# Kernel optimization log

Hardware: AMD Instinct MI355X
Metric: run time of the kernel (lower is better)

## Reference

```python
import jax, jax.numpy as jnp
import numpy as np

B, N, D, H = 4, 1024, 1024, 16
DH = D // H
MLP = 4 * D
EPS = 1e-6


def setup_inputs() -> dict:
    key = jax.random.key(0)
    ks = jax.random.split(key, 16)
    s = lambda fan_in: 1.0 / np.sqrt(fan_in)
    inp = {
        "x": jax.random.normal(ks[0], (B, N, D), jnp.float32),
        "c": jax.random.normal(ks[1], (B, D), jnp.float32),
        # weights stored (in, out); torch Linear is x @ W.T + b
        "Wq": jax.random.normal(ks[2], (D, D), jnp.float32) * s(D),
        "bq": jnp.zeros((D,), jnp.float32),
        "Wkv": jax.random.normal(ks[3], (D, 2 * D), jnp.float32) * s(D),
        "bkv": jnp.zeros((2 * D,), jnp.float32),
        "Wo": jax.random.normal(ks[4], (D, D), jnp.float32) * s(D),
        "bo": jnp.zeros((D,), jnp.float32),
        "W1": jax.random.normal(ks[5], (D, MLP), jnp.float32) * s(D),
        "b1": jnp.zeros((MLP,), jnp.float32),
        "W2": jax.random.normal(ks[6], (MLP, D), jnp.float32) * s(MLP),
        "b2": jnp.zeros((D,), jnp.float32),
        "Wada": jax.random.normal(ks[7], (D, 6 * D), jnp.float32) * s(D),
        "bada": jnp.zeros((6 * D,), jnp.float32),
    }
    return inp


def _layernorm(h):
    mu = jnp.mean(h, axis=-1, keepdims=True)
    var = jnp.mean(jnp.square(h - mu), axis=-1, keepdims=True)
    return (h - mu) / jnp.sqrt(var + EPS)


def _modulate(h, shift, scale):
    return h * (1.0 + scale[:, None, :]) + shift[:, None, :]


def reference(x, c, Wq, bq, Wkv, bkv, Wo, bo, W1, b1, W2, b2, Wada, bada):
    scale = DH ** -0.5
    mod = jax.nn.silu(c) @ Wada + bada  # [B, 6D]
    sh_msa, sc_msa, g_msa, sh_mlp, sc_mlp, g_mlp = jnp.split(mod, 6, axis=-1)

    # --- attention branch ---
    h = _modulate(_layernorm(x), sh_msa, sc_msa)
    q = (h @ Wq + bq).reshape(B, N, H, DH)
    kv = h @ Wkv + bkv
    k, v = jnp.split(kv, 2, axis=-1)
    k = k.reshape(B, N, H, DH)
    v = v.reshape(B, N, H, DH)
    sim = jnp.einsum("bihd,bjhd->bhij", q, k) * scale  # [B,H,N,N]
    attn = jax.nn.softmax(sim, axis=-1)
    out = jnp.einsum("bhij,bjhd->bihd", attn, v).reshape(B, N, D)
    out = out @ Wo + bo
    x = x + g_msa[:, None, :] * out

    # --- MLP branch ---
    h2 = _modulate(_layernorm(x), sh_mlp, sc_mlp)
    m = jax.nn.gelu(h2 @ W1 + b1, approximate=True) @ W2 + b2
    x = x + g_mlp[:, None, :] * m
    return x
```

## Files before the change

### kernel.cpp

```cpp
#include <hip/hip_runtime.h>
#include <hip/hip_bf16.h>
#include <cstdint>

typedef __attribute__((ext_vector_type(4))) float f32x4;
typedef __attribute__((ext_vector_type(16))) float f32x16;
typedef __attribute__((ext_vector_type(8))) short s16x8;
typedef __attribute__((ext_vector_type(4))) unsigned u32x4;
typedef unsigned short u16;

#define B_  4
#define N_  1024
#define D_  1024
#define H_  16
#define DH_ 64
#define M_  4096
#define SIXD 6144

__device__ __forceinline__ u16 f2bf(float f) {
    unsigned u = __builtin_bit_cast(unsigned, f);
    unsigned r = (u + 0x7fffu + ((u >> 16) & 1u)) >> 16;
    return (u16)r;
}

__device__ __forceinline__ unsigned cvtpk(float a, float b) {
    unsigned r;
    asm("v_cvt_pk_bf16_f32 %0, %1, %2" : "=v"(r) : "v"(a), "v"(b));
    return r;
}

__device__ __forceinline__ void gload16(const void* g, void* l) {
    __builtin_amdgcn_global_load_lds((const __attribute__((address_space(1))) void*)g,
                                     (__attribute__((address_space(3))) void*)l,
                                     16, 0, 0);
}

__global__ __launch_bounds__(256) void transpose_w(const float* __restrict__ in,
                                                   u16* __restrict__ out, int R, int C) {
    __shared__ float t[32][33];
    int tx = threadIdx.x & 31, ty = threadIdx.x >> 5;
    int r0 = blockIdx.y * 32, c0 = blockIdx.x * 32;
#pragma unroll
    for (int i = 0; i < 4; ++i)
        t[ty + 8 * i][tx] = in[(size_t)(r0 + ty + 8 * i) * C + c0 + tx];
    __syncthreads();
#pragma unroll
    for (int i = 0; i < 4; ++i)
        out[(size_t)(c0 + ty + 8 * i) * R + r0 + tx] = f2bf(t[tx][ty + 8 * i]);
}

__global__ __launch_bounds__(256) void modk(const float* __restrict__ c,
                                            const float* __restrict__ Wada,
                                            const float* __restrict__ bada,
                                            float* __restrict__ mod) {
    __shared__ float sc[D_];
    int b = blockIdx.y, tid = threadIdx.x;
    for (int i = tid; i < D_; i += 256) {
        float v = c[b * D_ + i];
        sc[i] = v / (1.f + __expf(-v));
    }
    __syncthreads();
    int col = blockIdx.x * 256 + tid;
    float a0 = 0.f, a1 = 0.f, a2 = 0.f, a3 = 0.f;
    for (int k = 0; k < D_; k += 4) {
        a0 = fmaf(sc[k + 0], Wada[(size_t)(k + 0) * SIXD + col], a0);
        a1 = fmaf(sc[k + 1], Wada[(size_t)(k + 1) * SIXD + col], a1);
        a2 = fmaf(sc[k + 2], Wada[(size_t)(k + 2) * SIXD + col], a2);
        a3 = fmaf(sc[k + 3], Wada[(size_t)(k + 3) * SIXD + col], a3);
    }
    mod[b * SIXD + col] = bada[col] + ((a0 + a1) + (a2 + a3));
}

__global__ __launch_bounds__(256) void ln_mod(const float* __restrict__ x,
                                              const float* __restrict__ mod,
                                              int shift_c, int scale_c,
                                              u16* __restrict__ h) {
    int row = blockIdx.x;
    int b = row >> 10;
    int tid = threadIdx.x, w = tid >> 6;
    float4 xv = ((const float4*)(x + (size_t)row * D_))[tid];
    float s  = xv.x + xv.y + xv.z + xv.w;
    float s2 = xv.x * xv.x + xv.y * xv.y + xv.z * xv.z + xv.w * xv.w;
#pragma unroll
    for (int m = 1; m <= 32; m <<= 1) { s += __shfl_xor(s, m); s2 += __shfl_xor(s2, m); }
    __shared__ float red[8];
    if ((tid & 63) == 0) { red[w * 2] = s; red[w * 2 + 1] = s2; }
    __syncthreads();
    float S  = red[0] + red[2] + red[4] + red[6];
    float S2 = red[1] + red[3] + red[5] + red[7];
    float mu = S * (1.f / D_);
    float var = S2 * (1.f / D_) - mu * mu;
    float rstd = rsqrtf(var + 1e-6f);
    int d0 = tid * 4;
    float4 shv = *(const float4*)(mod + b * SIXD + shift_c * D_ + d0);
    float4 scv = *(const float4*)(mod + b * SIXD + scale_c * D_ + d0);
    ushort4 o;
    o.x = f2bf((xv.x - mu) * rstd * (1.f + scv.x) + shv.x);
    o.y = f2bf((xv.y - mu) * rstd * (1.f + scv.y) + shv.y);
    o.z = f2bf((xv.z - mu) * rstd * (1.f + scv.z) + shv.z);
    o.w = f2bf((xv.w - mu) * rstd * (1.f + scv.w) + shv.w);
    *(ushort4*)(h + (size_t)row * D_ + d0) = o;
}

template <int EPI>
__global__ __launch_bounds__(256) void gemm_bt(const u16* __restrict__ A,
                                               const u16* __restrict__ Bt,
                                               const float* __restrict__ bias,
                                               const float* __restrict__ bias2,
                                               void* __restrict__ out,
                                               const float* __restrict__ xres,
                                               const float* __restrict__ mod,
                                               int M, int Nn, int K, int gate_c) {
    __shared__ char lds[2][32768];
    const int tid = threadIdx.x;
    const int w = tid >> 6, lane = tid & 63;
    const int li = lane & 15, lg = lane >> 4;
    const int nwg = gridDim.x * gridDim.y;
    const int flat = blockIdx.y * gridDim.x + blockIdx.x;
    const int wg = (flat & 7) * (nwg >> 3) + (flat >> 3);
    const int m0 = (wg / gridDim.x) * 128, n0 = (wg % gridDim.x) * 128;
    const int wr = w >> 1, wc = w & 1;

    f32x4 acc[4][4];
#pragma unroll
    for (int i = 0; i < 4; ++i)
#pragma unroll
        for (int j = 0; j < 4; ++j) acc[i][j] = (f32x4){0.f, 0.f, 0.f, 0.f};

    auto STAGE = [&](int kk, char* buf) {
#pragma unroll
        for (int j = 0; j < 8; ++j) {
            int basec = j * 256 + w * 64;
            int idx = basec + lane;
            int idl = idx & 1023;
            int row = idl >> 3, cc = idl & 7;
            const u16* src;
            if (idx < 1024)
                src = A + (size_t)(m0 + row) * K + kk + ((cc ^ (row & 7)) << 3);
            else
                src = Bt + (size_t)(n0 + row) * K + kk + ((cc ^ (row & 7)) << 3);
            gload16(src, buf + basec * 16);
        }
    };

    const int nt = K >> 6;
    STAGE(0, lds[0]);
    __syncthreads();
    int cur = 0;
    for (int t = 0; t < nt; ++t) {
        if (t + 1 < nt) STAGE((t + 1) << 6, lds[cur ^ 1]);
        const char* Ab = lds[cur];
        const char* Bb = lds[cur] + 16384;
#pragma unroll
        for (int hh = 0; hh < 2; ++hh) {
            s16x8 af[4], bfr[4];
#pragma unroll
            for (int mi = 0; mi < 4; ++mi) {
                int r = wr * 64 + mi * 16 + li;
                af[mi] = *(const s16x8*)(Ab + r * 128 + (((hh * 4 + lg) ^ (r & 7)) << 4));
            }
#pragma unroll
            for (int nj = 0; nj < 4; ++nj) {
                int r = wc * 64 + nj * 16 + li;
                bfr[nj] = *(const s16x8*)(Bb + r * 128 + (((hh * 4 + lg) ^ (r & 7)) << 4));
            }
#pragma unroll
            for (int mi = 0; mi < 4; ++mi)
#pragma unroll
                for (int nj = 0; nj < 4; ++nj)
                    acc[mi][nj] = __builtin_amdgcn_mfma_f32_16x16x32_bf16(
                        af[mi], bfr[nj], acc[mi][nj], 0, 0, 0);
        }
        __syncthreads();
        cur ^= 1;
    }

#pragma unroll
    for (int mi = 0; mi < 4; ++mi) {
#pragma unroll
        for (int nj = 0; nj < 4; ++nj) {
            int col = n0 + wc * 64 + nj * 16 + li;
            float bv;
            if (EPI == 5) bv = (col < D_) ? bias[col] : bias2[col - D_];
            else bv = bias[col];
#pragma unroll
            for (int rg = 0; rg < 4; ++rg) {
                int grow = m0 + wr * 64 + mi * 16 + 4 * lg + rg;
                float v = acc[mi][nj][rg] + bv;
                int b = grow >> 10, n = grow & 1023;
                if (EPI == 5) {
                    if (col < D_) {
                        int hd = col >> 6, dh = col & 63;
                        ((u16*)out)[(((size_t)(b * H_ + hd)) * N_ + n) * DH_ + dh] = f2bf(v);
                    } else if (col < 2 * D_) {
                        int c2 = col - D_;
                        int hd = c2 >> 6, dh = c2 & 63;
                        ((u16*)out)[4194304u + (((size_t)(b * H_ + hd)) * N_ + n) * DH_ + dh] =
                            f2bf(v);
                    } else {
                        int c2 = col - 2 * D_;
                        int hd = c2 >> 6, dh = c2 & 63;
                        ((u16*)out)[8388608u + (((size_t)(b * H_ + hd)) * DH_ + dh) * N_ + n] =
                            f2bf(v);
                    }
                } else if (EPI == 2 || EPI == 4) {
                    size_t off = (size_t)grow * D_ + col;
                    float g = mod[b * SIXD + gate_c * D_ + col];
                    ((float*)out)[off] = xres[off] + g * v;
                }
            }
        }
    }
}

__global__ __launch_bounds__(512, 2) void gemm256_gelu(const u16* __restrict__ A,
                                                       const u16* __restrict__ Bt,
                                                       const float* __restrict__ bias,
                                                       u16* __restrict__ out,
                                                       int M, int Nn, int K) {
    __shared__ char lds[2][65536];
    const int tid = threadIdx.x;
    const int w = tid >> 6, lane = tid & 63;
    const int li = lane & 15, lg = lane >> 4;
    const int wr = w >> 1, wc = w & 1;

    const int flat = blockIdx.x;
    const int wg = (flat & 7) * 32 + (flat >> 3);
    const int mg = wg >> 6, r_ = wg & 63;
    const int mt = mg * 4 + (r_ & 3), nt_ = r_ >> 2;
    const int m0 = mt * 256, n0 = nt_ * 256;

    f32x4 acc[4][8];
#pragma unroll
    for (int i = 0; i < 4; ++i)
#pragma unroll
        for (int j = 0; j < 8; ++j) acc[i][j] = (f32x4){0.f, 0.f, 0.f, 0.f};

    auto STAGE = [&](int kk, char* buf) {
#pragma unroll
        for (int j = 0; j < 4; ++j) {
            int basec = j * 512 + w * 64;
            int idx = basec + lane;
            int row = idx >> 3, cc = idx & 7;
            gload16(A + (size_t)(m0 + row) * K + kk + ((cc ^ (row & 7)) << 3),
                    buf + basec * 16);
            gload16(Bt + (size_t)(n0 + row) * K + kk + ((cc ^ (row & 7)) << 3),
                    buf + 32768 + basec * 16);
        }
    };

    const int nt = K >> 6;
    STAGE(0, lds[0]);
    __syncthreads();
    int cur = 0;
    for (int t = 0; t < nt; ++t) {
        if (t + 1 < nt) STAGE((t + 1) << 6, lds[cur ^ 1]);
        const char* Ab = lds[cur];
        const char* Bb = lds[cur] + 32768;
#pragma unroll
        for (int hh = 0; hh < 2; ++hh) {
            s16x8 af[4], bfr[8];
#pragma unroll
            for (int mi = 0; mi < 4; ++mi) {
                int r = wr * 64 + mi * 16 + li;
                af[mi] = *(const s16x8*)(Ab + r * 128 + (((hh * 4 + lg) ^ (r & 7)) << 4));
            }
#pragma unroll
            for (int nj = 0; nj < 8; ++nj) {
                int r = wc * 128 + nj * 16 + li;
                bfr[nj] = *(const s16x8*)(Bb + r * 128 + (((hh * 4 + lg) ^ (r & 7)) << 4));
            }
#pragma unroll
            for (int mi = 0; mi < 4; ++mi)
#pragma unroll
                for (int nj = 0; nj < 8; ++nj)
                    acc[mi][nj] = __builtin_amdgcn_mfma_f32_16x16x32_bf16(
                        af[mi], bfr[nj], acc[mi][nj], 0, 0, 0);
        }
        __syncthreads();
        cur ^= 1;
    }

#pragma unroll
    for (int nj = 0; nj < 8; ++nj) {
        int col = n0 + wc * 128 + nj * 16 + li;
        float bv = bias[col];
#pragma unroll
        for (int mi = 0; mi < 4; ++mi) {
#pragma unroll
            for (int rg = 0; rg < 4; ++rg) {
                int grow = m0 + wr * 64 + mi * 16 + 4 * lg + rg;
                float v = acc[mi][nj][rg] + bv;
                float u = 0.7978845608028654f * v * (1.f + 0.044715f * v * v);
                u = fminf(fmaxf(u, -15.f), 15.f);
                float e = __expf(2.f * u);
                float th = (e - 1.f) / (e + 1.f);
                out[(size_t)grow * (size_t)Nn + col] = f2bf(0.5f * v * (1.f + th));
            }
        }
    }
}

__global__ __launch_bounds__(256) void attn2(const u16* __restrict__ q,
                                             const u16* __restrict__ k,
                                             const u16* __restrict__ vt,
                                             u16* __restrict__ o) {
    __shared__ __align__(16) char qs[16384];
    __shared__ __align__(16) char kv[2][16384];
    const int tid = threadIdx.x, w = tid >> 6, lane = tid & 63;
    const int l31 = lane & 31, hi = lane >> 5;
    const int flat = blockIdx.x;
    const int wgs = (flat & 7) * 64 + (flat >> 3);
    const int bh = wgs >> 3, qt = wgs & 7;
    const size_t base = (size_t)bh * (N_ * DH_);
    const int q0 = qt * 128;

#pragma unroll
    for (int j = 0; j < 4; ++j) {
        int basec = j * 256 + w * 64;
        int idx = basec + lane;
        int row = idx >> 3, cc = idx & 7;
        gload16(q + base + (size_t)(q0 + row) * DH_ + ((cc ^ (row & 7)) << 3),
                qs + basec * 16);
    }
    auto STAGEKV = [&](int t, char* buf) {
#pragma unroll
        for (int j = 0; j < 4; ++j) {
            int basec = j * 256 + w * 64;
            int idx = basec + lane;
            if (idx < 512) {
                int row = idx >> 3, cc = idx & 7;
                gload16(k + base + (size_t)(t * 64 + row) * DH_ + ((cc ^ (row & 7)) << 3),
                        buf + basec * 16);
            } else {
                int i2 = idx - 512;
                int row = i2 >> 3, cc = i2 & 7;
                gload16(vt + base + (size_t)row * N_ + t * 64 + ((cc ^ (row & 7)) << 3),
                        buf + basec * 16);
            }
        }
    };
    STAGEKV(0, kv[0]);
    __syncthreads();

    s16x8 qf[4];
    const int qr = w * 32 + l31;
#pragma unroll
    for (int st = 0; st < 4; ++st)
        qf[st] = *(const s16x8*)(qs + qr * 128 + (((st * 2 + hi) ^ (qr & 7)) << 4));

    f32x16 oa[2];
#pragma unroll
    for (int r = 0; r < 16; ++r) { oa[0][r] = 0.f; oa[1][r] = 0.f; }
    float mrow = -3e38f, lrow = 0.f;
    const float CSC = 0.125f * 1.44269504088896f;

    int cur = 0;
    for (int t = 0; t < 16; ++t) {
        if (t + 1 < 16) STAGEKV(t + 1, kv[cur ^ 1]);
        const char* Kb = kv[cur];
        const char* Vb = kv[cur] + 8192;

        f32x16 s[2];
#pragma unroll
        for (int r = 0; r < 16; ++r) { s[0][r] = 0.f; s[1][r] = 0.f; }
#pragma unroll
        for (int st = 0; st < 4; ++st) {
#pragma unroll
            for (int ks = 0; ks < 2; ++ks) {
                int r = ks * 32 + l31;
                s16x8 ka = *(const s16x8*)(Kb + r * 128 + (((st * 2 + hi) ^ (r & 7)) << 4));
                s[ks] = __builtin_amdgcn_mfma_f32_32x32x16_bf16(ka, qf[st], s[ks], 0, 0, 0);
            }
        }

        float tmax = s[0][0];
#pragma unroll
        for (int r = 1; r < 16; ++r) tmax = fmaxf(tmax, s[0][r]);
#pragma unroll
        for (int r = 0; r < 16; ++r) tmax = fmaxf(tmax, s[1][r]);
        tmax = fmaxf(tmax, __shfl_xor(tmax, 32));
        float mn = fmaxf(mrow, tmax);
        float al = __builtin_amdgcn_exp2f((mrow - mn) * CSC);
        float nmc = -mn * CSC;
        float rs0 = 0.f, rs1 = 0.f;
#pragma unroll
        for (int r = 0; r < 16; ++r) {
            float p0 = __builtin_amdgcn_exp2f(fmaf(s[0][r], CSC, nmc));
            float p1 = __builtin_amdgcn_exp2f(fmaf(s[1][r], CSC, nmc));
            s[0][r] = p0; s[1][r] = p1;
            rs0 += p0; rs1 += p1;
        }
        float rs = rs0 + rs1;
        rs += __shfl_xor(rs, 32);
        lrow = lrow * al + rs;
        mrow = mn;
#pragma unroll
        for (int r = 0; r < 16; ++r) { oa[0][r] *= al; oa[1][r] *= al; }

        unsigned u[16];
#pragma unroll
        for (int ks = 0; ks < 2; ++ks)
#pragma unroll
            for (int j = 0; j < 4; ++j) {
                u[ks * 8 + 2 * j]     = cvtpk(s[ks][4 * j + 0], s[ks][4 * j + 1]);
                u[ks * 8 + 2 * j + 1] = cvtpk(s[ks][4 * j + 2], s[ks][4 * j + 3]);
            }

#pragma unroll
        for (int kstep = 0; kstep < 4; ++kstep) {
            unsigned b0 = u[kstep * 4 + 0], b1 = u[kstep * 4 + 1];
            unsigned b2 = u[kstep * 4 + 2], b3 = u[kstep * 4 + 3];
            asm volatile("v_permlane32_swap_b32 %0, %1" : "+v"(b0), "+v"(b2));
            asm volatile("v_permlane32_swap_b32 %0, %1" : "+v"(b1), "+v"(b3));
            u32x4 pbu = (u32x4){b0, b1, b2, b3};
            s16x8 pb = __builtin_bit_cast(s16x8, pbu);
#pragma unroll
            for (int ds = 0; ds < 2; ++ds) {
                int r = ds * 32 + l31;
                s16x8 va = *(const s16x8*)(Vb + r * 128 + (((kstep * 2 + hi) ^ (r & 7)) << 4));
                oa[ds] = __builtin_amdgcn_mfma_f32_32x32x16_bf16(va, pb, oa[ds], 0, 0, 0);
            }
        }
        __syncthreads();
        cur ^= 1;
    }

    float inv = 1.f / lrow;
#pragma unroll
    for (int ds = 0; ds < 2; ++ds)
#pragma unroll
        for (int j = 0; j < 4; ++j)
#pragma unroll
            for (int t2 = 0; t2 < 2; ++t2) {
                unsigned pk = cvtpk(oa[ds][4 * j + 2 * t2] * inv,
                                    oa[ds][4 * j + 2 * t2 + 1] * inv);
                int row = qr;
                int dch = 4 * ds + j;
                *(unsigned*)(qs + row * 128 + ((dch ^ (row & 7)) << 4) +
                             (4 * hi + 2 * t2) * 2) = pk;
            }
    __syncthreads();
    {
        int r = tid >> 1, h2 = tid & 1;
        const int b = bh >> 4, hd = bh & 15;
        size_t obase = ((size_t)(b * N_ + q0 + r)) * D_ + hd * DH_;
#pragma unroll
        for (int c = 0; c < 4; ++c) {
            int c2 = h2 * 4 + c;
            s16x8 v = *(const s16x8*)(qs + r * 128 + ((c2 ^ (r & 7)) << 4));
            *(s16x8*)(o + obase + c2 * 8) = v;
        }
    }
}

extern "C" void kernel_launch(void* const* d_in, const int* in_sizes, int n_in,
                              void* d_out, int out_size, void* d_ws, size_t ws_size,
                              hipStream_t stream) {
    const float* x    = (const float*)d_in[0];
    const float* c    = (const float*)d_in[1];
    const float* Wq   = (const float*)d_in[2];
    const float* bq   = (const float*)d_in[3];
    const float* Wkv  = (const float*)d_in[4];
    const float* bkv  = (const float*)d_in[5];
    const float* Wo   = (const float*)d_in[6];
    const float* bo   = (const float*)d_in[7];
    const float* W1   = (const float*)d_in[8];
    const float* b1   = (const float*)d_in[9];
    const float* W2   = (const float*)d_in[10];
    const float* b2   = (const float*)d_in[11];
    const float* Wada = (const float*)d_in[12];
    const float* bada = (const float*)d_in[13];

    char* ws = (char*)d_ws;
    const size_t MB = 1024 * 1024;
    u16*   wqkvT = (u16*)(ws + 0);
    u16*   woT  = (u16*)(ws + 6 * MB);
    u16*   w1T  = (u16*)(ws + 8 * MB);
    u16*   w2T  = (u16*)(ws + 16 * MB);
    float* mod  = (float*)(ws + 24 * MB);
    u16*   h    = (u16*)(ws + 25 * MB);
    u16*   qb   = (u16*)(ws + 33 * MB);
    u16*   ao   = (u16*)(ws + 57 * MB);
    float* x1   = (float*)(ws + 65 * MB);
    u16*   m1   = (u16*)(ws + 33 * MB);
    float* outp = (float*)d_out;

    transpose_w<<<dim3(32, 32), 256, 0, stream>>>(Wq, wqkvT, D_, D_);
    transpose_w<<<dim3(64, 32), 256, 0, stream>>>(Wkv, wqkvT + 1024 * 1024, D_, 2 * D_);
    transpose_w<<<dim3(32, 32), 256, 0, stream>>>(Wo, woT, D_, D_);
    transpose_w<<<dim3(128, 32), 256, 0, stream>>>(W1, w1T, D_, 4 * D_);
    transpose_w<<<dim3(32, 128), 256, 0, stream>>>(W2, w2T, 4 * D_, D_);

    modk<<<dim3(24, 4), 256, 0, stream>>>(c, Wada, bada, mod);
    ln_mod<<<M_, 256, 0, stream>>>(x, mod, 0, 1, h);

    gemm_bt<5><<<dim3(24, 32), 256, 0, stream>>>(h, wqkvT, bq, bkv, qb, nullptr, nullptr,
                                                 M_, 3 * D_, D_, 0);

    attn2<<<512, 256, 0, stream>>>(qb, qb + 4194304, qb + 8388608, ao);

    gemm_bt<2><<<dim3(8, 32), 256, 0, stream>>>(ao, woT, bo, nullptr, x1, x, mod,
                                                M_, D_, D_, 2);

    ln_mod<<<M_, 256, 0, stream>>>(x1, mod, 3, 4, h);

    gemm256_gelu<<<256, 512, 0, stream>>>(h, w1T, b1, m1, M_, 4 * D_, D_);
    gemm_bt<4><<<dim3(8, 32), 256, 0, stream>>>(m1, w2T, b2, nullptr, outp, x1, mod,
                                                M_, D_, 4 * D_, 5);
}
```

Before: 261.6 us.

## Merge weight transposes, move QKV to 256-tile GEMM, and relax pipeline waits

The five weight-transpose launches become a single kernel that picks its source matrix from the block index. The QKV projection moves from the 128-tile GEMM to a templated 256-tile GEMM, which gains an XCD-aware tile mapping and the head-layout epilogue. All GEMM and attention main loops replace __syncthreads with explicit vmcnt waits plus raw s_barrier, so the next stage's loads can stay in flight while the current tile is computed. This trims launch overhead and synchronization stalls, at the cost of relying on hand-counted vmcnt values being correct.

```diff
diff --git a/kernel.cpp b/kernel.cpp
--- a/kernel.cpp
+++ b/kernel.cpp
@@ -16,6 +16,8 @@
 #define M_  4096
 #define SIXD 6144
 
+#define WAITV(n) asm volatile("s_waitcnt vmcnt(" #n ")" ::: "memory")
+
 __device__ __forceinline__ u16 f2bf(float f) {
     unsigned u = __builtin_bit_cast(unsigned, f);
     unsigned r = (u + 0x7fffu + ((u >> 16) & 1u)) >> 16;
@@ -34,18 +36,34 @@
                                      16, 0, 0);
 }
 
-__global__ __launch_bounds__(256) void transpose_w(const float* __restrict__ in,
-                                                   u16* __restrict__ out, int R, int C) {
+__global__ __launch_bounds__(256) void transpose_all(const float* __restrict__ Wq,
+                                                     const float* __restrict__ Wkv,
+                                                     const float* __restrict__ Wo,
+                                                     const float* __restrict__ W1,
+                                                     const float* __restrict__ W2,
+                                                     u16* __restrict__ wqkvT,
+                                                     u16* __restrict__ woT,
+                                                     u16* __restrict__ w1T,
+                                                     u16* __restrict__ w2T) {
+    int id = blockIdx.x;
+    const float* in; u16* outp; int R, C, loc;
+    if (id < 1024)      { in = Wq;  outp = wqkvT;           R = 1024; C = 1024; loc = id; }
+    else if (id < 3072) { in = Wkv; outp = wqkvT + 1048576; R = 1024; C = 2048; loc = id - 1024; }
+    else if (id < 4096) { in = Wo;  outp = woT;             R = 1024; C = 1024; loc = id - 3072; }
+    else if (id < 8192) { in = W1;  outp = w1T;             R = 1024; C = 4096; loc = id - 4096; }
+    else                { in = W2;  outp = w2T;             R = 4096; C = 1024; loc = id - 8192; }
+    int tpc = C >> 5;
+    int bx = loc % tpc, by = loc / tpc;
     __shared__ float t[32][33];
     int tx = threadIdx.x & 31, ty = threadIdx.x >> 5;
-    int r0 = blockIdx.y * 32, c0 = blockIdx.x * 32;
+    int r0 = by * 32, c0 = bx * 32;
 #pragma unroll
     for (int i = 0; i < 4; ++i)
         t[ty + 8 * i][tx] = in[(size_t)(r0 + ty + 8 * i) * C + c0 + tx];
     __syncthreads();
 #pragma unroll
     for (int i = 0; i < 4; ++i)
-        out[(size_t)(c0 + ty + 8 * i) * R + r0 + tx] = f2bf(t[tx][ty + 8 * i]);
+        outp[(size_t)(c0 + ty + 8 * i) * R + r0 + tx] = f2bf(t[tx][ty + 8 * i]);
 }
 
 __global__ __launch_bounds__(256) void modk(const float* __restrict__ c,
@@ -105,7 +123,6 @@
 __global__ __launch_bounds__(256) void gemm_bt(const u16* __restrict__ A,
                                                const u16* __restrict__ Bt,
                                                const float* __restrict__ bias,
-                                               const float* __restrict__ bias2,
                                                void* __restrict__ out,
                                                const float* __restrict__ xres,
                                                const float* __restrict__ mod,
@@ -147,7 +164,10 @@
     __syncthreads();
     int cur = 0;
     for (int t = 0; t < nt; ++t) {
-        if (t + 1 < nt) STAGE((t + 1) << 6, lds[cur ^ 1]);
+        if (t + 1 < nt) { STAGE((t + 1) << 6, lds[cur ^ 1]); WAITV(8); }
+        else WAITV(0);
+        __builtin_amdgcn_s_barrier();
+        __builtin_amdgcn_sched_barrier(0);
         const char* Ab = lds[cur];
         const char* Bb = lds[cur] + 16384;
 #pragma unroll
@@ -170,7 +190,7 @@
                     acc[mi][nj] = __builtin_amdgcn_mfma_f32_16x16x32_bf16(
                         af[mi], bfr[nj], acc[mi][nj], 0, 0, 0);
         }
-        __syncthreads();
+        __builtin_amdgcn_s_barrier();
         cur ^= 1;
     }
 
@@ -179,44 +199,28 @@
 #pragma unroll
         for (int nj = 0; nj < 4; ++nj) {
             int col = n0 + wc * 64 + nj * 16 + li;
-            float bv;
-            if (EPI == 5) bv = (col < D_) ? bias[col] : bias2[col - D_];
-            else bv = bias[col];
+            float bv = bias[col];
 #pragma unroll
             for (int rg = 0; rg < 4; ++rg) {
                 int grow = m0 + wr * 64 + mi * 16 + 4 * lg + rg;
                 float v = acc[mi][nj][rg] + bv;
-                int b = grow >> 10, n = grow & 1023;
-                if (EPI == 5) {
-                    if (col < D_) {
-                        int hd = col >> 6, dh = col & 63;
-                        ((u16*)out)[(((size_t)(b * H_ + hd)) * N_ + n) * DH_ + dh] = f2bf(v);
-                    } else if (col < 2 * D_) {
-                        int c2 = col - D_;
-                        int hd = c2 >> 6, dh = c2 & 63;
-                        ((u16*)out)[4194304u + (((size_t)(b * H_ + hd)) * N_ + n) * DH_ + dh] =
-                            f2bf(v);
-                    } else {
-                        int c2 = col - 2 * D_;
-                        int hd = c2 >> 6, dh = c2 & 63;
-                        ((u16*)out)[8388608u + (((size_t)(b * H_ + hd)) * DH_ + dh) * N_ + n] =
-                            f2bf(v);
-                    }
-                } else if (EPI == 2 || EPI == 4) {
-                    size_t off = (size_t)grow * D_ + col;
-                    float g = mod[b * SIXD + gate_c * D_ + col];
-                    ((float*)out)[off] = xres[off] + g * v;
-                }
-            }
-        }
-    }
-}
-
-__global__ __launch_bounds__(512, 2) void gemm256_gelu(const u16* __restrict__ A,
-                                                       const u16* __restrict__ Bt,
-                                                       const float* __restrict__ bias,
-                                                       u16* __restrict__ out,
-                                                       int M, int Nn, int K) {
+                int b = grow >> 10;
+                size_t off = (size_t)grow * D_ + col;
+                float g = mod[b * SIXD + gate_c * D_ + col];
+                ((float*)out)[off] = xres[off] + g * v;
+            }
+        }
+    }
+}
+
+template <int EPI>
+__global__ __launch_bounds__(512, 2) void gemm256(const u16* __restrict__ A,
+                                                  const u16* __restrict__ Bt,
+                                                  const float* __restrict__ bias,
+                                                  const float* __restrict__ bias2,
+                                                  void* __restrict__ out,
+                                                  int M, int Nn, int K,
+                                                  int cm, int cn) {
     __shared__ char lds[2][65536];
     const int tid = threadIdx.x;
     const int w = tid >> 6, lane = tid & 63;
@@ -224,9 +228,11 @@
     const int wr = w >> 1, wc = w & 1;
 
     const int flat = blockIdx.x;
-    const int wg = (flat & 7) * 32 + (flat >> 3);
-    const int mg = wg >> 6, r_ = wg & 63;
-    const int mt = mg * 4 + (r_ & 3), nt_ = r_ >> 2;
+    const int xcd = flat & 7, r_ = flat >> 3;
+    const int ntn = Nn >> 8;
+    const int ncc = ntn / cn;
+    const int mt = (xcd / ncc) * cm + (r_ % cm);
+    const int nt_ = (xcd % ncc) * cn + (r_ / cm);
     const int m0 = mt * 256, n0 = nt_ * 256;
 
     f32x4 acc[4][8];
@@ -253,7 +259,10 @@
     __syncthreads();
     int cur = 0;
     for (int t = 0; t < nt; ++t) {
-        if (t + 1 < nt) STAGE((t + 1) << 6, lds[cur ^ 1]);
+        if (t + 1 < nt) { STAGE((t + 1) << 6, lds[cur ^ 1]); WAITV(8); }
+        else WAITV(0);
+        __builtin_amdgcn_s_barrier();
+        __builtin_amdgcn_sched_barrier(0);
         const char* Ab = lds[cur];
         const char* Bb = lds[cur] + 32768;
 #pragma unroll
@@ -276,25 +285,45 @@
                     acc[mi][nj] = __builtin_amdgcn_mfma_f32_16x16x32_bf16(
                         af[mi], bfr[nj], acc[mi][nj], 0, 0, 0);
         }
-        __syncthreads();
+        __builtin_amdgcn_s_barrier();
         cur ^= 1;
     }
 
 #pragma unroll
     for (int nj = 0; nj < 8; ++nj) {
         int col = n0 + wc * 128 + nj * 16 + li;
-        float bv = bias[col];
+        float bv;
+        if (EPI == 5) bv = (col < D_) ? bias[col] : bias2[col - D_];
+        else bv = bias[col];
 #pragma unroll
         for (int mi = 0; mi < 4; ++mi) {
 #pragma unroll
             for (int rg = 0; rg < 4; ++rg) {
                 int grow = m0 + wr * 64 + mi * 16 + 4 * lg + rg;
                 float v = acc[mi][nj][rg] + bv;
-                float u = 0.7978845608028654f * v * (1.f + 0.044715f * v * v);
-                u = fminf(fmaxf(u, -15.f), 15.f);
-                float e = __expf(2.f * u);
-                float th = (e - 1.f) / (e + 1.f);
-                out[(size_t)grow * (size_t)Nn + col] = f2bf(0.5f * v * (1.f + th));
+                if (EPI == 3) {
+                    float u = 0.7978845608028654f * v * (1.f + 0.044715f * v * v);
+                    u = fminf(fmaxf(u, -15.f), 15.f);
+                    float e = __expf(2.f * u);
+                    float th = (e - 1.f) / (e + 1.f);
+                    ((u16*)out)[(size_t)grow * (size_t)Nn + col] = f2bf(0.5f * v * (1.f + th));
+                } else {
+                    int b = grow >> 10, n = grow & 1023;
+                    if (n0 < 1024) {
+                        int hd = col >> 6, dh = col & 63;
+                        ((u16*)out)[(((size_t)(b * H_ + hd)) * N_ + n) * DH_ + dh] = f2bf(v);
+                    } else if (n0 < 2048) {
+                        int c2 = col - 1024;
+                        int hd = c2 >> 6, dh = c2 & 63;
+                        ((u16*)out)[4194304u + (((size_t)(b * H_ + hd)) * N_ + n) * DH_ + dh] =
+                            f2bf(v);
+                    } else {
+                        int c2 = col - 2048;
+                        int hd = c2 >> 6, dh = c2 & 63;
+                        ((u16*)out)[8388608u + (((size_t)(b * H_ + hd)) * DH_ + dh) * N_ + n] =
+                            f2bf(v);
+                    }
+                }
             }
         }
     }
@@ -356,7 +385,10 @@
 
     int cur = 0;
     for (int t = 0; t < 16; ++t) {
-        if (t + 1 < 16) STAGEKV(t + 1, kv[cur ^ 1]);
+        if (t + 1 < 16) { STAGEKV(t + 1, kv[cur ^ 1]); WAITV(4); }
+        else WAITV(0);
+        __builtin_amdgcn_s_barrier();
+        __builtin_amdgcn_sched_barrier(0);
         const char* Kb = kv[cur];
         const char* Vb = kv[cur] + 8192;
 
@@ -421,7 +453,7 @@
                 oa[ds] = __builtin_amdgcn_mfma_f32_32x32x16_bf16(va, pb, oa[ds], 0, 0, 0);
             }
         }
-        __syncthreads();
+        __builtin_amdgcn_s_barrier();
         cur ^= 1;
     }
 
@@ -485,26 +517,19 @@
     u16*   m1   = (u16*)(ws + 33 * MB);
     float* outp = (float*)d_out;
 
-    transpose_w<<<dim3(32, 32), 256, 0, stream>>>(Wq, wqkvT, D_, D_);
-    transpose_w<<<dim3(64, 32), 256, 0, stream>>>(Wkv, wqkvT + 1024 * 1024, D_, 2 * D_);
-    transpose_w<<<dim3(32, 32), 256, 0, stream>>>(Wo, woT, D_, D_);
-    transpose_w<<<dim3(128, 32), 256, 0, stream>>>(W1, w1T, D_, 4 * D_);
-    transpose_w<<<dim3(32, 128), 256, 0, stream>>>(W2, w2T, 4 * D_, D_);
+    transpose_all<<<12288, 256, 0, stream>>>(Wq, Wkv, Wo, W1, W2, wqkvT, woT, w1T, w2T);
 
     modk<<<dim3(24, 4), 256, 0, stream>>>(c, Wada, bada, mod);
     ln_mod<<<M_, 256, 0, stream>>>(x, mod, 0, 1, h);
 
-    gemm_bt<5><<<dim3(24, 32), 256, 0, stream>>>(h, wqkvT, bq, bkv, qb, nullptr, nullptr,
-                                                 M_, 3 * D_, D_, 0);
+    gemm256<5><<<192, 512, 0, stream>>>(h, wqkvT, bq, bkv, qb, M_, 3 * D_, D_, 4, 6);
 
     attn2<<<512, 256, 0, stream>>>(qb, qb + 4194304, qb + 8388608, ao);
 
-    gemm_bt<2><<<dim3(8, 32), 256, 0, stream>>>(ao, woT, bo, nullptr, x1, x, mod,
-                                                M_, D_, D_, 2);
+    gemm_bt<2><<<dim3(8, 32), 256, 0, stream>>>(ao, woT, bo, x1, x, mod, M_, D_, D_, 2);
 
     ln_mod<<<M_, 256, 0, stream>>>(x1, mod, 3, 4, h);
 
-    gemm256_gelu<<<256, 512, 0, stream>>>(h, w1T, b1, m1, M_, 4 * D_, D_);
-    gemm_bt<4><<<dim3(8, 32), 256, 0, stream>>>(m1, w2T, b2, nullptr, outp, x1, mod,
-                                                M_, D_, 4 * D_, 5);
-}
+    gemm256<3><<<256, 512, 0, stream>>>(h, w1T, b1, nullptr, m1, M_, 4 * D_, D_, 4, 8);
+    gemm_bt<4><<<dim3(8, 32), 256, 0, stream>>>(m1, w2T, b2, outp, x1, mod, M_, D_, 4 * D_, 5);
+}
```

After: 252.4 us. -3.5%, faster.
